# Performance work log

Hardware: AMD Instinct MI355X
Metric: run time of the kernel (lower is better)

Reference implementation:

```python
import jax, jax.numpy as jnp
import numpy as np

A = 384          # number of nodes
F = 128          # dim_feature
C = 32           # dim_outerproduct
NT = 4           # num_transition -> hidden = F*NT
EPS = 1e-5       # NORM_SMALL


def layer_norm(x, scale, bias, eps=EPS):
    mu = jnp.mean(x, axis=-1, keepdims=True)
    var = jnp.mean(jnp.square(x - mu), axis=-1, keepdims=True)
    return (x - mu) * jax.lax.rsqrt(var + eps) * scale + bias


def setup_inputs() -> dict:
    key = jax.random.key(0)
    ks = jax.random.split(key, 12)
    d = {
        "node_vec": jax.random.normal(ks[0], (A, F), dtype=jnp.float32),
        "edge_vec": jax.random.normal(ks[1], (A, A, F), dtype=jnp.float32),
        "node_mask": jnp.ones((A,), dtype=jnp.float32),
        "edge_mask": jnp.ones((A, A), dtype=jnp.float32),
        # OuterProduct params
        "op_ln_scale": jnp.ones((F,), jnp.float32),
        "op_ln_bias": jnp.zeros((F,), jnp.float32),
        "w_left": jax.random.normal(ks[2], (F, C), jnp.float32) / np.sqrt(F),
        "b_left": jnp.zeros((C,), jnp.float32),
        "w_right": jax.random.normal(ks[3], (F, C), jnp.float32) / np.sqrt(F),
        "b_right": jnp.zeros((C,), jnp.float32),
        "w_out": jax.random.normal(ks[4], (C * C, F), jnp.float32) / np.sqrt(C * C),
        "b_out": jnp.zeros((F,), jnp.float32),
        # Transition params
        "tr_ln_scale": jnp.ones((F,), jnp.float32),
        "tr_ln_bias": jnp.zeros((F,), jnp.float32),
        "w_t1": jax.random.normal(ks[5], (F, F * NT), jnp.float32) / np.sqrt(F),
        "b_t1": jnp.zeros((F * NT,), jnp.float32),
        "w_t2": jax.random.normal(ks[6], (F * NT, F), jnp.float32) / np.sqrt(F * NT),
        "b_t2": jnp.zeros((F,), jnp.float32),
    }
    return d


def reference(node_vec, edge_vec, node_mask, edge_mask,
              op_ln_scale, op_ln_bias, w_left, b_left, w_right, b_right,
              w_out, b_out, tr_ln_scale, tr_ln_bias, w_t1, b_t1, w_t2, b_t2):
    # ---- OuterProduct ----
    act = layer_norm(node_vec, op_ln_scale, op_ln_bias)          # [A, F]
    left = (act @ w_left + b_left) * node_mask[:, None]          # [A, C]
    right = (act @ w_right + b_right) * node_mask[:, None]       # [A, C]
    # original: [C*A,1] @ [1,A*C] -> reshape (C,A,A,C) -> transpose (1,2,0,3)
    # which is exactly op[a,b,c,d] = left[a,c] * right[b,d]
    op = jnp.einsum('ac,bd->abcd', left, right).reshape(A, A, C * C)
    op = op @ w_out + b_out                                      # [A, A, F]
    edge = edge_vec + op
    # ---- Transition (pre-norm MLP, relu) ----
    t = layer_norm(edge, tr_ln_scale, tr_ln_bias)
    t = jax.nn.relu(t @ w_t1 + b_t1)
    t = t @ w_t2 + b_t2
    return edge + t
```

## Files before the change

### kernel.cpp

```cpp
#include <hip/hip_runtime.h>
#include <stdint.h>
#include <stddef.h>

#define A_N 384
#define F_N 128
#define C_N 32
#define H_N 512
#define LN_EPS 1e-5f

typedef unsigned short u16;
typedef _Float16 f16;
typedef f16 f16x8 __attribute__((ext_vector_type(8)));
typedef float f32x4 __attribute__((ext_vector_type(4)));

__device__ float g_right[A_N * C_N];
__device__ f16   gLh[A_N * C_N];
__device__ f16   gMh[A_N * F_N * C_N];
__device__ int4  gW1P[16 * 512];
__device__ int4  gW2P[16 * 768];

__device__ __forceinline__ float b2f(u16 u) {
    union { float f; uint32_t i; } v; v.i = ((uint32_t)u) << 16; return v.f;
}
__device__ __forceinline__ float ld(const void* p, int idx, bool isbf) {
    if (isbf) return b2f(((const u16*)p)[idx]);
    return ((const float*)p)[idx];
}
__device__ __forceinline__ bool probe_bf16(const void* node_mask) {
    return ((const u16*)node_mask)[0] == 0x3F80u;
}
__device__ __forceinline__ f16x8 ldfrag(const void* p) {
    union { int4 i; f16x8 h; } u; u.i = *(const int4*)p; return u.h;
}
__device__ __forceinline__ void gload16(const void* gsrc, void* ldst) {
    __builtin_amdgcn_global_load_lds(
        (const __attribute__((address_space(1))) void*)gsrc,
        (__attribute__((address_space(3))) void*)ldst, 16, 0, 0);
}

__global__ void k_leftright(const void* __restrict__ node_vec, const void* __restrict__ node_mask,
                            const void* __restrict__ op_scale, const void* __restrict__ op_bias,
                            const void* __restrict__ w_left, const void* __restrict__ b_left,
                            const void* __restrict__ w_right, const void* __restrict__ b_right) {
    bool isbf = probe_bf16(node_mask);
    int a = blockIdx.x;
    int f = threadIdx.x;
    __shared__ float sAct[F_N];
    __shared__ float sRed[4];
    float x = ld(node_vec, a * F_N + f, isbf);
    float s1 = x, s2 = x * x;
    for (int o = 1; o < 64; o <<= 1) { s1 += __shfl_xor(s1, o); s2 += __shfl_xor(s2, o); }
    int wv = threadIdx.x >> 6;
    if ((threadIdx.x & 63) == 0) { sRed[wv * 2] = s1; sRed[wv * 2 + 1] = s2; }
    __syncthreads();
    float sum = sRed[0] + sRed[2], sq = sRed[1] + sRed[3];
    float mu = sum * (1.0f / F_N);
    float var = sq * (1.0f / F_N) - mu * mu;
    float rs = rsqrtf(var + LN_EPS);
    sAct[f] = (x - mu) * rs * ld(op_scale, f, isbf) + ld(op_bias, f, isbf);
    __syncthreads();
    if (threadIdx.x < 64) {
        int c = threadIdx.x & 31;
        bool isL = threadIdx.x < 32;
        const void* W = isL ? w_left : w_right;
        const void* B = isL ? b_left : b_right;
        float acc = ld(B, c, isbf);
        for (int ff = 0; ff < F_N; ff++) acc += sAct[ff] * ld(W, ff * C_N + c, isbf);
        acc *= ld(node_mask, a, isbf);
        if (isL) gLh[a * C_N + c] = (f16)acc;
        else     g_right[a * C_N + c] = acc;
    }
}

__global__ __launch_bounds__(256) void k_prep(const void* __restrict__ w_out,
                     const void* __restrict__ w_t1, const void* __restrict__ w_t2,
                     const void* __restrict__ node_mask) {
    bool isbf = probe_bf16(node_mask);
    const int t = threadIdx.x;
    if (blockIdx.x < 192) {
        __shared__ float sW[32 * F_N];
        __shared__ float sRl[8 * C_N];
        const int bg = blockIdx.x >> 2, cg = blockIdx.x & 3;
        const int b0 = bg * 8;
        sRl[t] = g_right[b0 * C_N + t];
        const int f = t & 127, bh = t >> 7;
        for (int ci = 0; ci < 8; ci++) {
            const int c = cg * 8 + ci;
            __syncthreads();
            if (isbf) {
                const int4* src = (const int4*)w_out + (size_t)c * 512;
                #pragma unroll
                for (int i = 0; i < 2; i++) {
                    union { int4 v; u16 h[8]; } u;
                    u.v = src[t + 256 * i];
                    #pragma unroll
                    for (int e = 0; e < 8; e++) sW[(t + 256 * i) * 8 + e] = b2f(u.h[e]);
                }
            } else {
                const int4* src = (const int4*)w_out + (size_t)c * 1024;
                #pragma unroll
                for (int i = 0; i < 4; i++)
                    ((int4*)sW)[t + 256 * i] = src[t + 256 * i];
            }
            __syncthreads();
            float acc[4] = {0.f, 0.f, 0.f, 0.f};
            for (int d = 0; d < 32; d++) {
                float w = sW[d * F_N + f];
                #pragma unroll
                for (int bb = 0; bb < 4; bb++)
                    acc[bb] += sRl[(bh * 4 + bb) * C_N + d] * w;
            }
            #pragma unroll
            for (int bb = 0; bb < 4; bb++) {
                int b = b0 + bh * 4 + bb;
                gMh[((size_t)b * F_N + f) * C_N + c] = (f16)acc[bb];
            }
        }
    } else if (blockIdx.x < 224) {
        int s = (blockIdx.x - 192) * 256 + t;
        int ch = s >> 9, r = s & 511, n = r >> 4, sgq = r & 15;
        int h = ch * 32 + n;
        union { int4 i; f16 hh[8]; } u;
        #pragma unroll
        for (int e = 0; e < 8; e++) u.hh[e] = (f16)ld(w_t1, (sgq * 8 + e) * H_N + h, isbf);
        gW1P[ch * 512 + n * 16 + (sgq ^ (n & 7))] = u.i;
    } else {
        int s = (blockIdx.x - 224) * 256 + t;
        int ch = s >> 9, r = s & 511, f = r >> 2, hb = r & 3;
        union { int4 i; f16 hh[8]; } u;
        #pragma unroll
        for (int e = 0; e < 8; e++) u.hh[e] = (f16)ld(w_t2, (ch * 32 + hb * 8 + e) * F_N + f, isbf);
        gW2P[(size_t)ch * 768 + f * 5 + hb] = u.i;
    }
}

#define SM_W1   0
#define SM_W2   16384
#define SM_RED  16384
#define SM_H    40960
#define SM_B1   46080
#define SM_SCL  48128
#define SM_BIA  48640
#define SM_B2   49152
#define SM_BOUT 49664
#define SM_TOT  50176

__global__ __launch_bounds__(256, 3) void k_fused(
    const void* __restrict__ edge_vec, const void* __restrict__ b_out,
    const void* __restrict__ tr_scale, const void* __restrict__ tr_bias,
    const void* __restrict__ b_t1, const void* __restrict__ b_t2,
    const void* __restrict__ node_mask, float* __restrict__ out)
{
    bool isbf = probe_bf16(node_mask);
    __shared__ __align__(16) unsigned char smem[SM_TOT];
    float* sRed   = (float*)(smem + SM_RED);
    float* sB1    = (float*)(smem + SM_B1);
    float* sScale = (float*)(smem + SM_SCL);
    float* sBias  = (float*)(smem + SM_BIA);
    float* sB2    = (float*)(smem + SM_B2);
    float* sBout  = (float*)(smem + SM_BOUT);

    const int t = threadIdx.x;
    const int lane = t & 63, wid = t >> 6;
    const int g = lane >> 4, fc = lane & 15;
    const int wr = wid >> 1, wc = wid & 1;

    const int L = blockIdx.x;
    const int xcd = L & 7, pos = L >> 3;
    const int bx = xcd * 12 + (pos % 12);
    const int by = pos / 12;
    const int a0 = by * 16, b0 = bx * 4;

    sB1[t]       = ld(b_t1, t, isbf);
    sB1[t + 256] = ld(b_t1, t + 256, isbf);
    if (t < 128) {
        sScale[t] = ld(tr_scale, t, isbf);
        sBias[t]  = ld(tr_bias, t, isbf);
        sB2[t]    = ld(b_t2, t, isbf);
        sBout[t]  = ld(b_out, t, isbf);
    }
    __syncthreads();

    f32x4 acc2[2][4];
    const f32x4 zero4 = (f32x4){0.f, 0.f, 0.f, 0.f};
    f16x8 aL = ldfrag(gLh + (a0 + fc) * C_N + g * 8);
    #pragma unroll
    for (int bb = 0; bb < 2; bb++) {
        int b = b0 + wr * 2 + bb;
        #pragma unroll
        for (int nc = 0; nc < 4; nc++) {
            int f = wc * 64 + nc * 16 + fc;
            f16x8 bM = ldfrag(gMh + ((size_t)(b * F_N + f)) * C_N + g * 8);
            acc2[bb][nc] = __builtin_amdgcn_mfma_f32_16x16x32_f16(aL, bM, zero4, 0, 0, 0);
        }
    }
    #pragma unroll
    for (int bb = 0; bb < 2; bb++) {
        int b = b0 + wr * 2 + bb;
        #pragma unroll
        for (int nc = 0; nc < 4; nc++) {
            int f = wc * 64 + nc * 16 + fc;
            float bo = sBout[f];
            #pragma unroll
            for (int rg = 0; rg < 4; rg++) {
                int a = a0 + g * 4 + rg;
                acc2[bb][nc][rg] += ld(edge_vec, (a * A_N + b) * F_N + f, isbf) + bo;
            }
        }
    }
    float pA[2][4], qA[2][4];
    #pragma unroll
    for (int bb = 0; bb < 2; bb++)
        #pragma unroll
        for (int rg = 0; rg < 4; rg++) {
            float e0 = acc2[bb][0][rg], e1 = acc2[bb][1][rg];
            float e2 = acc2[bb][2][rg], e3 = acc2[bb][3][rg];
            float p = e0 + e1 + e2 + e3;
            float q = e0 * e0 + e1 * e1 + e2 * e2 + e3 * e3;
            p += __shfl_xor(p, 1); q += __shfl_xor(q, 1);
            p += __shfl_xor(p, 2); q += __shfl_xor(q, 2);
            p += __shfl_xor(p, 4); q += __shfl_xor(q, 4);
            p += __shfl_xor(p, 8); q += __shfl_xor(q, 8);
            pA[bb][rg] = p; qA[bb][rg] = q;
            if (fc == 0) {
                int r = wr * 32 + bb * 16 + g * 4 + rg;
                sRed[r * 4 + wc * 2]     = p;
                sRed[r * 4 + wc * 2 + 1] = q;
            }
        }
    __syncthreads();
    float muA[2][4], rsA[2][4];
    #pragma unroll
    for (int bb = 0; bb < 2; bb++)
        #pragma unroll
        for (int rg = 0; rg < 4; rg++) {
            int r = wr * 32 + bb * 16 + g * 4 + rg;
            float s1 = pA[bb][rg] + sRed[r * 4 + (wc ^ 1) * 2];
            float s2 = qA[bb][rg] + sRed[r * 4 + (wc ^ 1) * 2 + 1];
            float mu = s1 * (1.0f / F_N);
            float var = s2 * (1.0f / F_N) - mu * mu;
            muA[bb][rg] = mu;
            rsA[bb][rg] = rsqrtf(var + LN_EPS);
        }
    #pragma unroll
    for (int bb = 0; bb < 2; bb++)
        #pragma unroll
        for (int nc = 0; nc < 4; nc++) {
            int f = wc * 64 + nc * 16 + fc;
            float sc = sScale[f], bi = sBias[f];
            #pragma unroll
            for (int rg = 0; rg < 4; rg++) {
                int r = wr * 32 + bb * 16 + g * 4 + rg;
                float x = (acc2[bb][nc][rg] - muA[bb][rg]) * rsA[bb][rg] * sc + bi;
                *(f16*)(smem + r * 256 + ((f * 2) ^ ((r & 7) << 4))) = (f16)x;
            }
        }
    __syncthreads();

    f16x8 a1[2][4];
    #pragma unroll
    for (int mr = 0; mr < 2; mr++)
        #pragma unroll
        for (int ks = 0; ks < 4; ks++) {
            int r = wr * 32 + mr * 16 + fc;
            a1[mr][ks] = ldfrag(smem + r * 256 + ((ks * 64 + g * 16) ^ ((r & 7) << 4)));
        }
    __syncthreads();

    {
        #pragma unroll
        for (int i = 0; i < 2; i++) {
            int s = i * 4 + wid;
            gload16(gW1P + 0 * 512 + s * 64 + lane, smem + SM_W1 + 0 * 8192 + s * 1024);
        }
        #pragma unroll
        for (int i = 0; i < 3; i++) {
            int s = i * 4 + wid;
            gload16(gW2P + (size_t)0 * 768 + s * 64 + lane, smem + SM_W2 + 0 * 12288 + s * 1024);
        }
    }
    __syncthreads();

    for (int ch = 0; ch < 16; ch++) {
        const int cur = ch & 1;
        const int h0 = ch * 32;

        if (ch < 15) {
            const int nxt = cur ^ 1;
            #pragma unroll
            for (int i = 0; i < 2; i++) {
                int s = i * 4 + wid;
                gload16(gW1P + (ch + 1) * 512 + s * 64 + lane,
                        smem + SM_W1 + nxt * 8192 + s * 1024);
            }
            #pragma unroll
            for (int i = 0; i < 3; i++) {
                int s = i * 4 + wid;
                gload16(gW2P + (size_t)(ch + 1) * 768 + s * 64 + lane,
                        smem + SM_W2 + nxt * 12288 + s * 1024);
            }
        }

        f32x4 acc1[2];
        acc1[0] = zero4; acc1[1] = zero4;
        __builtin_amdgcn_s_setprio(1);
        #pragma unroll
        for (int ks = 0; ks < 4; ks++) {
            int n = wc * 16 + fc;
            f16x8 bfr = ldfrag(smem + SM_W1 + cur * 8192 + n * 256 +
                               ((ks * 64 + g * 16) ^ ((n & 7) << 4)));
            #pragma unroll
            for (int mr = 0; mr < 2; mr++)
                acc1[mr] = __builtin_amdgcn_mfma_f32_16x16x32_f16(a1[mr][ks], bfr, acc1[mr], 0, 0, 0);
        }
        __builtin_amdgcn_s_setprio(0);
        {
            int jl = wc * 16 + fc;
            float b1v = sB1[h0 + jl];
            #pragma unroll
            for (int mr = 0; mr < 2; mr++)
                #pragma unroll
                for (int rg = 0; rg < 4; rg++) {
                    int r2 = wr * 32 + mr * 16 + g * 4 + rg;
                    *(f16*)(smem + SM_H + r2 * 80 + jl * 2) =
                        (f16)fmaxf(acc1[mr][rg] + b1v, 0.f);
                }
        }
        __syncthreads();

        __builtin_amdgcn_s_setprio(1);
        {
            f16x8 afr2[2], bfr2[4];
            #pragma unroll
            for (int mr = 0; mr < 2; mr++) {
                int r = wr * 32 + mr * 16 + fc;
                afr2[mr] = ldfrag(smem + SM_H + r * 80 + g * 16);
            }
            #pragma unroll
            for (int nc = 0; nc < 4; nc++) {
                int fR = wc * 64 + nc * 16 + fc;
                bfr2[nc] = ldfrag(smem + SM_W2 + cur * 12288 + fR * 80 + g * 16);
            }
            #pragma unroll
            for (int mr = 0; mr < 2; mr++)
                #pragma unroll
                for (int nc = 0; nc < 4; nc++)
                    acc2[mr][nc] = __builtin_amdgcn_mfma_f32_16x16x32_f16(
                        afr2[mr], bfr2[nc], acc2[mr][nc], 0, 0, 0);
        }
        __builtin_amdgcn_s_setprio(0);
        __syncthreads();
    }

    #pragma unroll
    for (int bb = 0; bb < 2; bb++) {
        int b = b0 + wr * 2 + bb;
        #pragma unroll
        for (int nc = 0; nc < 4; nc++) {
            int f = wc * 64 + nc * 16 + fc;
            float b2v = sB2[f];
            #pragma unroll
            for (int rg = 0; rg < 4; rg++) {
                int a = a0 + g * 4 + rg;
                out[((size_t)a * A_N + b) * F_N + f] = acc2[bb][nc][rg] + b2v;
            }
        }
    }
}

extern "C" void kernel_launch(void* const* d_in, const int* in_sizes, int n_in,
                              void* d_out, int out_size, void* d_ws, size_t ws_size,
                              hipStream_t stream) {
    const void* node_vec  = d_in[0];
    const void* edge_vec  = d_in[1];
    const void* node_mask = d_in[2];
    const void* op_scale  = d_in[4];
    const void* op_bias   = d_in[5];
    const void* w_left    = d_in[6];
    const void* b_left    = d_in[7];
    const void* w_right   = d_in[8];
    const void* b_right   = d_in[9];
    const void* w_out     = d_in[10];
    const void* b_out     = d_in[11];
    const void* tr_scale  = d_in[12];
    const void* tr_bias   = d_in[13];
    const void* w_t1      = d_in[14];
    const void* b_t1      = d_in[15];
    const void* w_t2      = d_in[16];
    const void* b_t2      = d_in[17];
    float* out = (float*)d_out;
    (void)d_ws; (void)ws_size; (void)in_sizes; (void)n_in; (void)out_size;

    hipLaunchKernelGGL(k_leftright, dim3(A_N), dim3(128), 0, stream,
                       node_vec, node_mask, op_scale, op_bias,
                       w_left, b_left, w_right, b_right);
    hipLaunchKernelGGL(k_prep, dim3(256), dim3(256), 0, stream,
                       w_out, w_t1, w_t2, node_mask);
    hipLaunchKernelGGL(k_fused, dim3(2304), dim3(256), 0, stream,
                       edge_vec, b_out, tr_scale, tr_bias, b_t1, b_t2, node_mask, out);
}
```

Baseline: 268.5 us.

## Compute right-by-w_out projection with MFMA and merge prep kernels

```diff
diff --git a/kernel.cpp b/kernel.cpp
--- a/kernel.cpp
+++ b/kernel.cpp
@@ -13,8 +13,9 @@
 typedef f16 f16x8 __attribute__((ext_vector_type(8)));
 typedef float f32x4 __attribute__((ext_vector_type(4)));
 
-__device__ float g_right[A_N * C_N];
 __device__ f16   gLh[A_N * C_N];
+__device__ f16   gRh[A_N * C_N];
+__device__ f16   gWoT[F_N * C_N * C_N];
 __device__ f16   gMh[A_N * F_N * C_N];
 __device__ int4  gW1P[16 * 512];
 __device__ int4  gW2P[16 * 768];
@@ -38,99 +39,94 @@
         (__attribute__((address_space(3))) void*)ldst, 16, 0, 0);
 }
 
-__global__ void k_leftright(const void* __restrict__ node_vec, const void* __restrict__ node_mask,
-                            const void* __restrict__ op_scale, const void* __restrict__ op_bias,
-                            const void* __restrict__ w_left, const void* __restrict__ b_left,
-                            const void* __restrict__ w_right, const void* __restrict__ b_right) {
-    bool isbf = probe_bf16(node_mask);
-    int a = blockIdx.x;
-    int f = threadIdx.x;
-    __shared__ float sAct[F_N];
-    __shared__ float sRed[4];
-    float x = ld(node_vec, a * F_N + f, isbf);
-    float s1 = x, s2 = x * x;
-    for (int o = 1; o < 64; o <<= 1) { s1 += __shfl_xor(s1, o); s2 += __shfl_xor(s2, o); }
-    int wv = threadIdx.x >> 6;
-    if ((threadIdx.x & 63) == 0) { sRed[wv * 2] = s1; sRed[wv * 2 + 1] = s2; }
-    __syncthreads();
-    float sum = sRed[0] + sRed[2], sq = sRed[1] + sRed[3];
-    float mu = sum * (1.0f / F_N);
-    float var = sq * (1.0f / F_N) - mu * mu;
-    float rs = rsqrtf(var + LN_EPS);
-    sAct[f] = (x - mu) * rs * ld(op_scale, f, isbf) + ld(op_bias, f, isbf);
-    __syncthreads();
-    if (threadIdx.x < 64) {
-        int c = threadIdx.x & 31;
-        bool isL = threadIdx.x < 32;
-        const void* W = isL ? w_left : w_right;
-        const void* B = isL ? b_left : b_right;
-        float acc = ld(B, c, isbf);
-        for (int ff = 0; ff < F_N; ff++) acc += sAct[ff] * ld(W, ff * C_N + c, isbf);
-        acc *= ld(node_mask, a, isbf);
-        if (isL) gLh[a * C_N + c] = (f16)acc;
-        else     g_right[a * C_N + c] = acc;
-    }
-}
-
-__global__ __launch_bounds__(256) void k_prep(const void* __restrict__ w_out,
-                     const void* __restrict__ w_t1, const void* __restrict__ w_t2,
-                     const void* __restrict__ node_mask) {
+__global__ __launch_bounds__(128) void k_pre(
+    const void* __restrict__ node_vec, const void* __restrict__ node_mask,
+    const void* __restrict__ op_scale, const void* __restrict__ op_bias,
+    const void* __restrict__ w_left, const void* __restrict__ b_left,
+    const void* __restrict__ w_right, const void* __restrict__ b_right,
+    const void* __restrict__ w_out, const void* __restrict__ w_t1,
+    const void* __restrict__ w_t2) {
     bool isbf = probe_bf16(node_mask);
     const int t = threadIdx.x;
-    if (blockIdx.x < 192) {
-        __shared__ float sW[32 * F_N];
-        __shared__ float sRl[8 * C_N];
-        const int bg = blockIdx.x >> 2, cg = blockIdx.x & 3;
-        const int b0 = bg * 8;
-        sRl[t] = g_right[b0 * C_N + t];
-        const int f = t & 127, bh = t >> 7;
-        for (int ci = 0; ci < 8; ci++) {
-            const int c = cg * 8 + ci;
-            __syncthreads();
-            if (isbf) {
-                const int4* src = (const int4*)w_out + (size_t)c * 512;
-                #pragma unroll
-                for (int i = 0; i < 2; i++) {
-                    union { int4 v; u16 h[8]; } u;
-                    u.v = src[t + 256 * i];
-                    #pragma unroll
-                    for (int e = 0; e < 8; e++) sW[(t + 256 * i) * 8 + e] = b2f(u.h[e]);
-                }
-            } else {
-                const int4* src = (const int4*)w_out + (size_t)c * 1024;
-                #pragma unroll
-                for (int i = 0; i < 4; i++)
-                    ((int4*)sW)[t + 256 * i] = src[t + 256 * i];
-            }
-            __syncthreads();
-            float acc[4] = {0.f, 0.f, 0.f, 0.f};
-            for (int d = 0; d < 32; d++) {
-                float w = sW[d * F_N + f];
-                #pragma unroll
-                for (int bb = 0; bb < 4; bb++)
-                    acc[bb] += sRl[(bh * 4 + bb) * C_N + d] * w;
-            }
-            #pragma unroll
-            for (int bb = 0; bb < 4; bb++) {
-                int b = b0 + bh * 4 + bb;
-                gMh[((size_t)b * F_N + f) * C_N + c] = (f16)acc[bb];
-            }
-        }
-    } else if (blockIdx.x < 224) {
-        int s = (blockIdx.x - 192) * 256 + t;
+    if (blockIdx.x < 384) {
+        __shared__ float sAct[F_N];
+        __shared__ float sRed[4];
+        int a = blockIdx.x;
+        int f = t;
+        float x = ld(node_vec, a * F_N + f, isbf);
+        float s1 = x, s2 = x * x;
+        for (int o = 1; o < 64; o <<= 1) { s1 += __shfl_xor(s1, o); s2 += __shfl_xor(s2, o); }
+        int wv = t >> 6;
+        if ((t & 63) == 0) { sRed[wv * 2] = s1; sRed[wv * 2 + 1] = s2; }
+        __syncthreads();
+        float sum = sRed[0] + sRed[2], sq = sRed[1] + sRed[3];
+        float mu = sum * (1.0f / F_N);
+        float var = sq * (1.0f / F_N) - mu * mu;
+        float rs = rsqrtf(var + LN_EPS);
+        sAct[f] = (x - mu) * rs * ld(op_scale, f, isbf) + ld(op_bias, f, isbf);
+        __syncthreads();
+        if (t < 64) {
+            int c = t & 31;
+            bool isL = t < 32;
+            const void* W = isL ? w_left : w_right;
+            const void* B = isL ? b_left : b_right;
+            float acc = ld(B, c, isbf);
+            for (int ff = 0; ff < F_N; ff++) acc += sAct[ff] * ld(W, ff * C_N + c, isbf);
+            acc *= ld(node_mask, a, isbf);
+            if (isL) gLh[a * C_N + c] = (f16)acc;
+            else     gRh[a * C_N + c] = (f16)acc;
+        }
+    } else if (blockIdx.x < 448) {
+        int s = (blockIdx.x - 384) * 128 + t;
         int ch = s >> 9, r = s & 511, n = r >> 4, sgq = r & 15;
         int h = ch * 32 + n;
         union { int4 i; f16 hh[8]; } u;
         #pragma unroll
         for (int e = 0; e < 8; e++) u.hh[e] = (f16)ld(w_t1, (sgq * 8 + e) * H_N + h, isbf);
         gW1P[ch * 512 + n * 16 + (sgq ^ (n & 7))] = u.i;
-    } else {
-        int s = (blockIdx.x - 224) * 256 + t;
+    } else if (blockIdx.x < 512) {
+        int s = (blockIdx.x - 448) * 128 + t;
         int ch = s >> 9, r = s & 511, f = r >> 2, hb = r & 3;
         union { int4 i; f16 hh[8]; } u;
         #pragma unroll
         for (int e = 0; e < 8; e++) u.hh[e] = (f16)ld(w_t2, (ch * 32 + hb * 8 + e) * F_N + f, isbf);
         gW2P[(size_t)ch * 768 + f * 5 + hb] = u.i;
+    } else {
+        int row = (blockIdx.x - 512) * 128 + t;
+        int c = row & 31, f = row >> 5;
+        union { int4 i4[4]; f16 h[32]; } u;
+        #pragma unroll
+        for (int d = 0; d < 32; d++) u.h[d] = (f16)ld(w_out, (c * 32 + d) * F_N + f, isbf);
+        int4* dst = (int4*)(gWoT + (size_t)row * 32);
+        dst[0] = u.i4[0]; dst[1] = u.i4[1]; dst[2] = u.i4[2]; dst[3] = u.i4[3];
+    }
+}
+
+__global__ __launch_bounds__(256) void k_mgemm() {
+    const int t = threadIdx.x;
+    const int lane = t & 63, wid = t >> 6;
+    const int g = lane >> 4, fc = lane & 15;
+    const int bw = wid >> 1, cw = wid & 1;
+    const int bg = blockIdx.x >> 4, fg = blockIdx.x & 15;
+    const int b0w = bg * 32 + bw * 16;
+    const int fc0 = fg * 256 + cw * 128;
+    const f32x4 zero4 = (f32x4){0.f, 0.f, 0.f, 0.f};
+
+    f16x8 afr = ldfrag(gRh + (b0w + fc) * C_N + g * 8);
+    f32x4 acc[8];
+    #pragma unroll
+    for (int nc = 0; nc < 8; nc++) {
+        f16x8 bfr = ldfrag(gWoT + (size_t)(fc0 + nc * 16 + fc) * 32 + g * 8);
+        acc[nc] = __builtin_amdgcn_mfma_f32_16x16x32_f16(afr, bfr, zero4, 0, 0, 0);
+    }
+    #pragma unroll
+    for (int nc = 0; nc < 8; nc++) {
+        int col = fc0 + nc * 16 + fc;
+        #pragma unroll
+        for (int rg = 0; rg < 4; rg++) {
+            int b = b0w + g * 4 + rg;
+            gMh[(size_t)b * 4096 + col] = (f16)acc[nc][rg];
+        }
     }
 }
 
@@ -391,11 +387,10 @@
     float* out = (float*)d_out;
     (void)d_ws; (void)ws_size; (void)in_sizes; (void)n_in; (void)out_size;
 
-    hipLaunchKernelGGL(k_leftright, dim3(A_N), dim3(128), 0, stream,
+    hipLaunchKernelGGL(k_pre, dim3(544), dim3(128), 0, stream,
                        node_vec, node_mask, op_scale, op_bias,
-                       w_left, b_left, w_right, b_right);
-    hipLaunchKernelGGL(k_prep, dim3(256), dim3(256), 0, stream,
-                       w_out, w_t1, w_t2, node_mask);
+                       w_left, b_left, w_right, b_right, w_out, w_t1, w_t2);
+    hipLaunchKernelGGL(k_mgemm, dim3(192), dim3(256), 0, stream);
     hipLaunchKernelGGL(k_fused, dim3(2304), dim3(256), 0, stream,
                        edge_vec, b_out, tr_scale, tr_bias, b_t1, b_t2, node_mask, out);
 }
```

Result: faster. 250.3 us (-6.8%).
